# Performance work log

Hardware: AMD Instinct MI355X
Metric: run time of the kernel (lower is better)

## Reference

```python
import jax, jax.numpy as jnp
import numpy as np

N_NODES = 50000
N_EDGES = 800000
N_GRAPHS = 64
IN_C = 256      # num_commodities
HID = 256       # hidden_units
HID2 = HID // 2
N_DCS = 64


def setup_inputs() -> dict:
    key = jax.random.key(0)
    ks = jax.random.split(key, 8)
    x = jax.random.normal(ks[0], (N_NODES, IN_C), dtype=jnp.float32)
    edge_index = jax.random.randint(ks[1], (2, N_EDGES), 0, N_NODES, dtype=jnp.int32)
    # sorted graph-membership ids; even partition guarantees no empty graph
    batch = ((jnp.arange(N_NODES) * N_GRAPHS) // N_NODES).astype(jnp.int32)
    s1 = 1.0 / np.sqrt(IN_C)
    s2 = 1.0 / np.sqrt(HID)
    s3 = 1.0 / np.sqrt(HID2)
    W1 = jax.random.normal(ks[2], (IN_C, HID), dtype=jnp.float32) * s1
    b1 = jnp.zeros((HID,), dtype=jnp.float32)
    W2 = jax.random.normal(ks[3], (HID, HID2), dtype=jnp.float32) * s2
    b2 = jnp.zeros((HID2,), dtype=jnp.float32)
    Wm = jax.random.normal(ks[4], (HID2, N_DCS), dtype=jnp.float32) * s3
    bm = jax.random.normal(ks[5], (N_DCS,), dtype=jnp.float32) * s3
    return {"x": x, "edge_index": edge_index, "batch": batch,
            "W1": W1, "b1": b1, "W2": W2, "b2": b2, "Wm": Wm, "bm": bm}


def gcn_conv(x, W, b, src, dst, n_nodes):
    """PyG GCNConv: D^{-1/2}(A+I)D^{-1/2} X W + b (self-loops added)."""
    h = x @ W                                    # [N, out]
    ones = jnp.ones(src.shape[0], dtype=h.dtype)
    deg = jax.ops.segment_sum(ones, dst, num_segments=n_nodes) + 1.0  # +1 self-loop
    dis = jax.lax.rsqrt(deg)                     # deg >= 1, safe
    norm = dis[src] * dis[dst]                   # [E]
    agg = jax.ops.segment_sum(h[src] * norm[:, None], dst, num_segments=n_nodes)
    agg = agg + h * (dis * dis)[:, None]         # self-loop contribution
    return agg + b


def reference(x, edge_index, batch, W1, b1, W2, b2, Wm, bm):
    src, dst = edge_index[0], edge_index[1]
    n = x.shape[0]
    bx = jax.nn.relu(gcn_conv(x, W1, b1, src, dst, n))
    cx = jax.nn.relu(gcn_conv(bx, W2, b2, src, dst, n))
    px = jax.ops.segment_max(cx, batch, num_segments=N_GRAPHS)  # global max pool
    return px @ Wm + bm                           # [N_GRAPHS, N_DCS]
```

## Files before the change

kernel.cpp:

```cpp
#include <hip/hip_runtime.h>
#include <cstdint>


typedef _Float16 half2v __attribute__((ext_vector_type(2)));
typedef _Float16 half4v __attribute__((ext_vector_type(4)));
typedef _Float16 half8v __attribute__((ext_vector_type(8)));
typedef float f32x4 __attribute__((ext_vector_type(4)));

#define CAP 64

__device__ __forceinline__ void gl_lds16(const void* g, void* l) {
  __builtin_amdgcn_global_load_lds(
      (const __attribute__((address_space(1))) unsigned int*)g,
      (__attribute__((address_space(3))) unsigned int*)l, 16, 0, 0);
}

__global__ void cvtW_k(const float* __restrict__ W1, _Float16* __restrict__ Wt1,
                       const float* __restrict__ W2, _Float16* __restrict__ Wt2) {
  int i = blockIdx.x * 256 + threadIdx.x;
  if (i < 256 * 256) {
    int k = i >> 8, c = i & 255;
    Wt1[c * 256 + k] = (_Float16)W1[i];
  } else {
    int j = i - 256 * 256;
    if (j < 256 * 128) {
      int k = j >> 7, c = j & 127;
      Wt2[c * 256 + k] = (_Float16)W2[j];
    }
  }
}

__global__ void fill_slots_k(const int* __restrict__ src, const int* __restrict__ dst,
                             int* __restrict__ cnt, unsigned short* __restrict__ slots,
                             int E) {
  int e = blockIdx.x * blockDim.x + threadIdx.x;
  if (e >= E) return;
  int d = dst[e];
  int s = src[e];
  int p = atomicAdd(&cnt[d << 4], 1);
  if (p < CAP) slots[(d << 6) + p] = (unsigned short)s;
}

__global__ __launch_bounds__(256) void gemm1_k(const float* __restrict__ A,
                                               const _Float16* __restrict__ Bt,
                                               const int* __restrict__ cnt,
                                               _Float16* __restrict__ C, int M) {
  constexpr int K = 256, N = 256, BM = 32, BK = 32;
  __shared__ _Float16 As[BM * BK];
  __shared__ _Float16 Bs[N * BK];
  const int tid = threadIdx.x, lane = tid & 63, wave = tid >> 6;
  const int row0 = blockIdx.x * BM;
  const int kbase = (lane >> 4) * 8;
  const int r16 = lane & 15;

  const _Float16* bSrc[4];
  _Float16* bDst[4];
#pragma unroll
  for (int hh = 0; hh < 4; ++hh) {
    int fl = hh * 4 + wave;
    bSrc[hh] = Bt + (size_t)(fl * 16 + r16) * K + kbase;
    bDst[hh] = Bs + fl * 512;
  }

  const bool doA = tid < 128;
  const float* aSrc = nullptr;
  _Float16* aDst = nullptr;
  if (doA) {
    int arow = row0 + (tid >> 2);
    if (arow > M - 1) arow = M - 1;
    aSrc = A + (size_t)arow * K + (tid & 3) * 8;
    aDst = As + (tid >> 6) * 512 + (((tid & 3) << 4) + ((tid >> 2) & 15)) * 8;
  }

  f32x4 acc[2][4] = {};
  for (int k0 = 0; k0 < K; k0 += BK) {
#pragma unroll
    for (int hh = 0; hh < 4; ++hh) gl_lds16(bSrc[hh] + k0, bDst[hh]);
    if (doA) {
      float4 a0 = *(const float4*)(aSrc + k0);
      float4 a1 = *(const float4*)(aSrc + k0 + 4);
      half8v ah = {(_Float16)a0.x, (_Float16)a0.y, (_Float16)a0.z, (_Float16)a0.w,
                   (_Float16)a1.x, (_Float16)a1.y, (_Float16)a1.z, (_Float16)a1.w};
      *(half8v*)aDst = ah;
    }
    __syncthreads();

    half8v af[2], bf[4];
#pragma unroll
    for (int m = 0; m < 2; ++m)
      af[m] = *(const half8v*)(As + m * 512 + lane * 8);
#pragma unroll
    for (int nj = 0; nj < 4; ++nj)
      bf[nj] = *(const half8v*)(Bs + (wave * 4 + nj) * 512 + lane * 8);
#pragma unroll
    for (int m = 0; m < 2; ++m)
#pragma unroll
      for (int nj = 0; nj < 4; ++nj)
        acc[m][nj] = __builtin_amdgcn_mfma_f32_16x16x32_f16(af[m], bf[nj], acc[m][nj], 0, 0, 0);
    __syncthreads();
  }

#pragma unroll
  for (int m = 0; m < 2; ++m) {
    const int rbase = row0 + m * 16 + (lane >> 4) * 4;
    float dr[4];
#pragma unroll
    for (int r = 0; r < 4; ++r)
      dr[r] = (rbase + r < M) ? rsqrtf((float)cnt[(rbase + r) << 4] + 1.0f) : 0.f;
#pragma unroll
    for (int nj = 0; nj < 4; ++nj) {
      int col = wave * 64 + nj * 16 + r16;
#pragma unroll
      for (int r = 0; r < 4; ++r) {
        int row = rbase + r;
        if (row < M) C[(size_t)row * N + col] = (_Float16)(acc[m][nj][r] * dr[r]);
      }
    }
  }
}

__global__ __launch_bounds__(256) void gemm2_k(const _Float16* __restrict__ A,
                                               const _Float16* __restrict__ Bt,
                                               const int* __restrict__ cnt,
                                               _Float16* __restrict__ C, int M) {
  constexpr int K = 256, N = 128, BM = 32, BK = 32;
  __shared__ _Float16 As[BM * BK];
  __shared__ _Float16 Bs[N * BK];
  const int tid = threadIdx.x, lane = tid & 63, wave = tid >> 6;
  const int row0 = blockIdx.x * BM;
  const int kbase = (lane >> 4) * 8;
  const int r16 = lane & 15;

  const _Float16* bSrc[2];
  _Float16* bDst[2];
#pragma unroll
  for (int hh = 0; hh < 2; ++hh) {
    int fl = hh * 4 + wave;
    bSrc[hh] = Bt + (size_t)(fl * 16 + r16) * K + kbase;
    bDst[hh] = Bs + fl * 512;
  }

  const _Float16* aSrc = nullptr;
  _Float16* aDst = nullptr;
  if (wave < 2) {
    int arow = row0 + wave * 16 + r16;
    if (arow > M - 1) arow = M - 1;
    aSrc = A + (size_t)arow * K + kbase;
    aDst = As + wave * 512;
  }

  f32x4 acc[2][2] = {};
  for (int k0 = 0; k0 < K; k0 += BK) {
    gl_lds16(bSrc[0] + k0, bDst[0]);
    gl_lds16(bSrc[1] + k0, bDst[1]);
    if (wave < 2) gl_lds16(aSrc + k0, aDst);
    __syncthreads();

    half8v af[2], bf[2];
#pragma unroll
    for (int m = 0; m < 2; ++m)
      af[m] = *(const half8v*)(As + m * 512 + lane * 8);
#pragma unroll
    for (int j = 0; j < 2; ++j)
      bf[j] = *(const half8v*)(Bs + (wave * 2 + j) * 512 + lane * 8);
#pragma unroll
    for (int m = 0; m < 2; ++m)
#pragma unroll
      for (int j = 0; j < 2; ++j)
        acc[m][j] = __builtin_amdgcn_mfma_f32_16x16x32_f16(af[m], bf[j], acc[m][j], 0, 0, 0);
    __syncthreads();
  }

#pragma unroll
  for (int m = 0; m < 2; ++m) {
    const int rbase = row0 + m * 16 + (lane >> 4) * 4;
    float dr[4];
#pragma unroll
    for (int r = 0; r < 4; ++r)
      dr[r] = (rbase + r < M) ? rsqrtf((float)cnt[(rbase + r) << 4] + 1.0f) : 0.f;
#pragma unroll
    for (int j = 0; j < 2; ++j) {
      int col = wave * 32 + j * 16 + r16;
#pragma unroll
      for (int r = 0; r < 4; ++r) {
        int row = rbase + r;
        if (row < M) C[(size_t)row * N + col] = (_Float16)(acc[m][j][r] * dr[r]);
      }
    }
  }
}

template <int C, bool POOL>
__global__ __launch_bounds__(256) void agg_k(const _Float16* __restrict__ h,
                                             const int* __restrict__ cnt,
                                             const unsigned short* __restrict__ slots,
                                             const float* __restrict__ bias,
                                             const int* __restrict__ batch,
                                             void* __restrict__ outv, int n) {
  constexpr int LPR = C / 8;
  constexpr int EPW = 64 / LPR;
  constexpr int U = 8;
  constexpr int EBLK = EPW * U;
  const int tid = threadIdx.x;
  const int lane = tid & 63;
  const int wave = tid >> 6;
  const int slot = lane / LPR;
  const int ch0 = (lane % LPR) * 8;

  const int wid = blockIdx.x * 4 + wave;
  const bool valid = wid < n;
  const int node = valid ? wid : n - 1;

  const int rawc = cnt[node << 4];
  const int end = rawc < CAP ? rawc : CAP;
  const unsigned short* nsl = slots + (node << 6);

  float acc[8] = {};
  int jb = 0;
  for (; jb + EBLK <= end; jb += EBLK) {
    half2v ah0[4] = {}, ah1[4] = {};
#pragma unroll
    for (int u = 0; u < U; ++u) {
      int s = nsl[jb + u * EPW + slot];
      half8v hv = *(const half8v*)(h + (size_t)s * C + ch0);
      const half2v* hp = (const half2v*)&hv;
      if (u < 4) {
#pragma unroll
        for (int p = 0; p < 4; ++p) ah0[p] += hp[p];
      } else {
#pragma unroll
        for (int p = 0; p < 4; ++p) ah1[p] += hp[p];
      }
    }
#pragma unroll
    for (int p = 0; p < 4; ++p) {
      acc[2 * p + 0] += (float)ah0[p][0] + (float)ah1[p][0];
      acc[2 * p + 1] += (float)ah0[p][1] + (float)ah1[p][1];
    }
  }
  if (jb < end) {
    half2v ah0[4] = {}, ah1[4] = {};
#pragma unroll
    for (int u = 0; u < U; ++u) {
      int e = jb + u * EPW + slot;
      bool ok = e < end;
      int s = nsl[ok ? e : end - 1];
      half8v hv = *(const half8v*)(h + (size_t)s * C + ch0);
      if (!ok) hv = half8v{};
      const half2v* hp = (const half2v*)&hv;
      if (u < 4) {
#pragma unroll
        for (int p = 0; p < 4; ++p) ah0[p] += hp[p];
      } else {
#pragma unroll
        for (int p = 0; p < 4; ++p) ah1[p] += hp[p];
      }
    }
#pragma unroll
    for (int p = 0; p < 4; ++p) {
      acc[2 * p + 0] += (float)ah0[p][0] + (float)ah1[p][0];
      acc[2 * p + 1] += (float)ah0[p][1] + (float)ah1[p][1];
    }
  }

  if constexpr (EPW == 4) {
#pragma unroll
    for (int v = 0; v < 8; ++v) {
      acc[v] += __shfl_xor(acc[v], 16);
      acc[v] += __shfl_xor(acc[v], 32);
    }
  } else {
#pragma unroll
    for (int v = 0; v < 8; ++v) acc[v] += __shfl_xor(acc[v], 32);
  }

  const float di = rsqrtf((float)rawc + 1.0f);
  half8v sv = *(const half8v*)(h + (size_t)node * C + ch0);
  float4 blo = *(const float4*)(bias + ch0);
  float4 bhi = *(const float4*)(bias + ch0 + 4);
  const float bb[8] = {blo.x, blo.y, blo.z, blo.w, bhi.x, bhi.y, bhi.z, bhi.w};
  float res[8];
#pragma unroll
  for (int v = 0; v < 8; ++v)
    res[v] = fmaxf((acc[v] + (float)sv[v]) * di + bb[v], 0.f);

  if constexpr (!POOL) {
    if (valid && lane < LPR) {
      half8v r;
#pragma unroll
      for (int v = 0; v < 8; ++v) r[v] = (_Float16)res[v];
      *(half8v*)((_Float16*)outv + (size_t)node * C + ch0) = r;
    }
  } else {
    __shared__ float pres[4][C];
    __shared__ int pg[4];
    __shared__ int uni;
    const int g = valid ? batch[node] : -1 - wave;
    if (lane < LPR) {
      *(f32x4*)&pres[wave][ch0] = f32x4{res[0], res[1], res[2], res[3]};
      *(f32x4*)&pres[wave][ch0 + 4] = f32x4{res[4], res[5], res[6], res[7]};
    }
    if (lane == 0) pg[wave] = g;
    __syncthreads();
    if (tid == 0) uni = (pg[0] == pg[1] && pg[1] == pg[2] && pg[2] == pg[3] && pg[0] >= 0);
    __syncthreads();
    float* px = (float*)outv;
    if (uni) {
      if (tid < C) {
        float m = fmaxf(fmaxf(pres[0][tid], pres[1][tid]),
                        fmaxf(pres[2][tid], pres[3][tid]));
        atomicMax((int*)&px[(size_t)pg[0] * C + tid], __float_as_int(m));
      }
    } else {
#pragma unroll
      for (int wv = 0; wv < 4; ++wv) {
        int gg = pg[wv];
        if (gg >= 0 && tid < C)
          atomicMax((int*)&px[(size_t)gg * C + tid], __float_as_int(pres[wv][tid]));
      }
    }
  }
}

__global__ void final_mm_k(const float* __restrict__ px, const float* __restrict__ Wm,
                           const float* __restrict__ bm, float* __restrict__ out) {
  int g = blockIdx.x;
  int c = threadIdx.x;
  float acc = bm[c];
#pragma unroll 8
  for (int k = 0; k < 128; ++k)
    acc = fmaf(px[g * 128 + k], Wm[k * 64 + c], acc);
  out[g * 64 + c] = acc;
}

extern "C" void kernel_launch(void* const* d_in, const int* in_sizes, int n_in,
                              void* d_out, int out_size, void* d_ws, size_t ws_size,
                              hipStream_t stream) {
  const float* x     = (const float*)d_in[0];
  const int*   ei    = (const int*)d_in[1];
  const int*   batch = (const int*)d_in[2];
  const float* W1    = (const float*)d_in[3];
  const float* b1    = (const float*)d_in[4];
  const float* W2    = (const float*)d_in[5];
  const float* b2    = (const float*)d_in[6];
  const float* Wm    = (const float*)d_in[7];
  const float* bm    = (const float*)d_in[8];
  float* out = (float*)d_out;

  const int E = in_sizes[1] / 2;
  const int n = in_sizes[2];
  const int HID = 256, HID2 = 128, NG = 64;
  const int* src = ei;
  const int* dst = ei + E;

  char* w = (char*)d_ws;
  size_t off = 0;
  auto alloc = [&](size_t bytes) -> void* {
    void* p = w + off;
    off = (off + bytes + 255) & ~(size_t)255;
    return p;
  };
  int*            cnt    = (int*)alloc((size_t)n * 16 * 4);
  float*          px     = (float*)alloc((size_t)NG * HID2 * 4);
  size_t          zlen   = off;
  unsigned short* slots  = (unsigned short*)alloc((size_t)n * CAP * 2);
  _Float16*       Wt1    = (_Float16*)alloc((size_t)HID * 256 * 2);
  _Float16*       Wt2    = (_Float16*)alloc((size_t)HID2 * HID * 2);
  _Float16*       bufA   = (_Float16*)alloc((size_t)n * HID * 2);
  _Float16*       bufB   = (_Float16*)alloc((size_t)n * HID * 2);
  _Float16* h1 = bufA;
  _Float16* bx = bufB;
  _Float16* h2 = bufA;

  hipMemsetAsync(cnt, 0, zlen, stream);

  cvtW_k<<<(256 * 256 + 256 * 128 + 255) / 256, 256, 0, stream>>>(W1, Wt1, W2, Wt2);
  fill_slots_k<<<(E + 255) / 256, 256, 0, stream>>>(src, dst, cnt, slots, E);

  gemm1_k<<<(n + 31) / 32, 256, 0, stream>>>(x, Wt1, cnt, h1, n);
  agg_k<256, false><<<(n + 3) / 4, 256, 0, stream>>>(h1, cnt, slots, b1, nullptr, bx, n);

  gemm2_k<<<(n + 31) / 32, 256, 0, stream>>>(bx, Wt2, cnt, h2, n);
  agg_k<128, true><<<(n + 3) / 4, 256, 0, stream>>>(h2, cnt, slots, b2, batch, px, n);

  final_mm_k<<<NG, 64, 0, stream>>>(px, Wm, bm, out);
}
```

Measured before the change: 309.6 us.

## Store features in 32-channel column slices to shrink gather working set

GEMM outputs are now written in a channel-grouped layout, with each 32-channel slice stored contiguously for all nodes. Aggregation blocks each handle one slice, so random neighbour gathers touch only a per-slice working set (about 3.2MB) that fits in cache. Degree norms and clamped counts are precomputed into compact dis32/cnt8 arrays to avoid repeated rsqrt and strided count reads. The cost is more blocks, shorter 64-byte gathers, four-step shuffle reductions per node per slice, repeated slot-list reads per slice, and less coalesced GEMM output stores.

```diff
diff --git a/kernel.cpp b/kernel.cpp
--- a/kernel.cpp
+++ b/kernel.cpp
@@ -44,10 +44,13 @@
 __global__ __launch_bounds__(256) void gemm1_k(const float* __restrict__ A,
                                                const _Float16* __restrict__ Bt,
                                                const int* __restrict__ cnt,
-                                               _Float16* __restrict__ C, int M) {
-  constexpr int K = 256, N = 256, BM = 32, BK = 32;
+                                               _Float16* __restrict__ Cg,
+                                               float* __restrict__ dis32,
+                                               unsigned char* __restrict__ cnt8,
+                                               int M) {
+  constexpr int K = 256, BM = 32, BK = 32;
   __shared__ _Float16 As[BM * BK];
-  __shared__ _Float16 Bs[N * BK];
+  __shared__ _Float16 Bs[256 * BK];
   const int tid = threadIdx.x, lane = tid & 63, wave = tid >> 6;
   const int row0 = blockIdx.x * BM;
   const int kbase = (lane >> 4) * 8;
@@ -107,25 +110,38 @@
 #pragma unroll
     for (int r = 0; r < 4; ++r)
       dr[r] = (rbase + r < M) ? rsqrtf((float)cnt[(rbase + r) << 4] + 1.0f) : 0.f;
+    if (r16 == 0 && wave == 0) {
+#pragma unroll
+      for (int r = 0; r < 4; ++r) {
+        int row = rbase + r;
+        if (row < M) {
+          int rc = cnt[row << 4];
+          dis32[row] = dr[r];
+          cnt8[row] = (unsigned char)(rc < CAP ? rc : CAP);
+        }
+      }
+    }
 #pragma unroll
     for (int nj = 0; nj < 4; ++nj) {
       int col = wave * 64 + nj * 16 + r16;
+      int g = col >> 5, cg = col & 31;
 #pragma unroll
       for (int r = 0; r < 4; ++r) {
         int row = rbase + r;
-        if (row < M) C[(size_t)row * N + col] = (_Float16)(acc[m][nj][r] * dr[r]);
-      }
-    }
-  }
-}
-
-__global__ __launch_bounds__(256) void gemm2_k(const _Float16* __restrict__ A,
+        if (row < M)
+          Cg[((size_t)g * M + row) * 32 + cg] = (_Float16)(acc[m][nj][r] * dr[r]);
+      }
+    }
+  }
+}
+
+__global__ __launch_bounds__(256) void gemm2_k(const _Float16* __restrict__ Ag,
                                                const _Float16* __restrict__ Bt,
-                                               const int* __restrict__ cnt,
-                                               _Float16* __restrict__ C, int M) {
-  constexpr int K = 256, N = 128, BM = 32, BK = 32;
+                                               const float* __restrict__ dis32,
+                                               _Float16* __restrict__ Cg, int M) {
+  constexpr int K = 256, BM = 32, BK = 32;
   __shared__ _Float16 As[BM * BK];
-  __shared__ _Float16 Bs[N * BK];
+  __shared__ _Float16 Bs[128 * BK];
   const int tid = threadIdx.x, lane = tid & 63, wave = tid >> 6;
   const int row0 = blockIdx.x * BM;
   const int kbase = (lane >> 4) * 8;
@@ -140,12 +156,11 @@
     bDst[hh] = Bs + fl * 512;
   }
 
-  const _Float16* aSrc = nullptr;
+  int arow = 0;
   _Float16* aDst = nullptr;
   if (wave < 2) {
-    int arow = row0 + wave * 16 + r16;
+    arow = row0 + wave * 16 + r16;
     if (arow > M - 1) arow = M - 1;
-    aSrc = A + (size_t)arow * K + kbase;
     aDst = As + wave * 512;
   }
 
@@ -153,7 +168,8 @@
   for (int k0 = 0; k0 < K; k0 += BK) {
     gl_lds16(bSrc[0] + k0, bDst[0]);
     gl_lds16(bSrc[1] + k0, bDst[1]);
-    if (wave < 2) gl_lds16(aSrc + k0, aDst);
+    if (wave < 2)
+      gl_lds16(Ag + ((size_t)(k0 >> 5) * M + arow) * 32 + kbase, aDst);
     __syncthreads();
 
     half8v af[2], bf[2];
@@ -176,108 +192,68 @@
     const int rbase = row0 + m * 16 + (lane >> 4) * 4;
     float dr[4];
 #pragma unroll
-    for (int r = 0; r < 4; ++r)
-      dr[r] = (rbase + r < M) ? rsqrtf((float)cnt[(rbase + r) << 4] + 1.0f) : 0.f;
+    for (int r = 0; r < 4; ++r) dr[r] = (rbase + r < M) ? dis32[rbase + r] : 0.f;
 #pragma unroll
     for (int j = 0; j < 2; ++j) {
       int col = wave * 32 + j * 16 + r16;
+      int g = col >> 5, cg = col & 31;
 #pragma unroll
       for (int r = 0; r < 4; ++r) {
         int row = rbase + r;
-        if (row < M) C[(size_t)row * N + col] = (_Float16)(acc[m][j][r] * dr[r]);
-      }
-    }
-  }
-}
-
-template <int C, bool POOL>
-__global__ __launch_bounds__(256) void agg_k(const _Float16* __restrict__ h,
-                                             const int* __restrict__ cnt,
+        if (row < M)
+          Cg[((size_t)g * M + row) * 32 + cg] = (_Float16)(acc[m][j][r] * dr[r]);
+      }
+    }
+  }
+}
+
+template <int NGRP, bool POOL>
+__global__ __launch_bounds__(256) void agg_k(const _Float16* __restrict__ hg,
+                                             const float* __restrict__ dis32,
+                                             const unsigned char* __restrict__ cnt8,
                                              const unsigned short* __restrict__ slots,
                                              const float* __restrict__ bias,
                                              const int* __restrict__ batch,
                                              void* __restrict__ outv, int n) {
-  constexpr int LPR = C / 8;
-  constexpr int EPW = 64 / LPR;
-  constexpr int U = 8;
-  constexpr int EBLK = EPW * U;
   const int tid = threadIdx.x;
   const int lane = tid & 63;
   const int wave = tid >> 6;
-  const int slot = lane / LPR;
-  const int ch0 = (lane % LPR) * 8;
-
-  const int wid = blockIdx.x * 4 + wave;
+  const int g = blockIdx.x & (NGRP - 1);
+  const int chunk = blockIdx.x / NGRP;
+  const int slot = lane >> 2;
+  const int c8 = (lane & 3) * 8;
+
+  const int wid = chunk * 4 + wave;
   const bool valid = wid < n;
   const int node = valid ? wid : n - 1;
 
-  const int rawc = cnt[node << 4];
-  const int end = rawc < CAP ? rawc : CAP;
+  const int end = cnt8[node];
   const unsigned short* nsl = slots + (node << 6);
+  const _Float16* hslice = hg + (size_t)g * n * 32;
 
   float acc[8] = {};
-  int jb = 0;
-  for (; jb + EBLK <= end; jb += EBLK) {
-    half2v ah0[4] = {}, ah1[4] = {};
-#pragma unroll
-    for (int u = 0; u < U; ++u) {
-      int s = nsl[jb + u * EPW + slot];
-      half8v hv = *(const half8v*)(h + (size_t)s * C + ch0);
-      const half2v* hp = (const half2v*)&hv;
-      if (u < 4) {
-#pragma unroll
-        for (int p = 0; p < 4; ++p) ah0[p] += hp[p];
-      } else {
-#pragma unroll
-        for (int p = 0; p < 4; ++p) ah1[p] += hp[p];
-      }
-    }
-#pragma unroll
-    for (int p = 0; p < 4; ++p) {
-      acc[2 * p + 0] += (float)ah0[p][0] + (float)ah1[p][0];
-      acc[2 * p + 1] += (float)ah0[p][1] + (float)ah1[p][1];
-    }
-  }
-  if (jb < end) {
-    half2v ah0[4] = {}, ah1[4] = {};
-#pragma unroll
-    for (int u = 0; u < U; ++u) {
-      int e = jb + u * EPW + slot;
-      bool ok = e < end;
-      int s = nsl[ok ? e : end - 1];
-      half8v hv = *(const half8v*)(h + (size_t)s * C + ch0);
-      if (!ok) hv = half8v{};
-      const half2v* hp = (const half2v*)&hv;
-      if (u < 4) {
-#pragma unroll
-        for (int p = 0; p < 4; ++p) ah0[p] += hp[p];
-      } else {
-#pragma unroll
-        for (int p = 0; p < 4; ++p) ah1[p] += hp[p];
-      }
-    }
-#pragma unroll
-    for (int p = 0; p < 4; ++p) {
-      acc[2 * p + 0] += (float)ah0[p][0] + (float)ah1[p][0];
-      acc[2 * p + 1] += (float)ah0[p][1] + (float)ah1[p][1];
-    }
-  }
-
-  if constexpr (EPW == 4) {
-#pragma unroll
-    for (int v = 0; v < 8; ++v) {
-      acc[v] += __shfl_xor(acc[v], 16);
-      acc[v] += __shfl_xor(acc[v], 32);
-    }
-  } else {
-#pragma unroll
-    for (int v = 0; v < 8; ++v) acc[v] += __shfl_xor(acc[v], 32);
-  }
-
-  const float di = rsqrtf((float)rawc + 1.0f);
-  half8v sv = *(const half8v*)(h + (size_t)node * C + ch0);
-  float4 blo = *(const float4*)(bias + ch0);
-  float4 bhi = *(const float4*)(bias + ch0 + 4);
+  for (int jb = 0; jb < end; jb += 16) {
+    int e = jb + slot;
+    bool ok = e < end;
+    int s = nsl[ok ? e : 0];
+    half8v hv = *(const half8v*)(hslice + (size_t)s * 32 + c8);
+    if (!ok) hv = half8v{};
+#pragma unroll
+    for (int v = 0; v < 8; ++v) acc[v] += (float)hv[v];
+  }
+
+#pragma unroll
+  for (int v = 0; v < 8; ++v) {
+    acc[v] += __shfl_xor(acc[v], 4);
+    acc[v] += __shfl_xor(acc[v], 8);
+    acc[v] += __shfl_xor(acc[v], 16);
+    acc[v] += __shfl_xor(acc[v], 32);
+  }
+
+  const float di = dis32[node];
+  half8v sv = *(const half8v*)(hslice + (size_t)node * 32 + c8);
+  float4 blo = *(const float4*)(bias + g * 32 + c8);
+  float4 bhi = *(const float4*)(bias + g * 32 + c8 + 4);
   const float bb[8] = {blo.x, blo.y, blo.z, blo.w, bhi.x, bhi.y, bhi.z, bhi.w};
   float res[8];
 #pragma unroll
@@ -285,38 +261,39 @@
     res[v] = fmaxf((acc[v] + (float)sv[v]) * di + bb[v], 0.f);
 
   if constexpr (!POOL) {
-    if (valid && lane < LPR) {
+    if (valid && lane < 4) {
       half8v r;
 #pragma unroll
       for (int v = 0; v < 8; ++v) r[v] = (_Float16)res[v];
-      *(half8v*)((_Float16*)outv + (size_t)node * C + ch0) = r;
+      *(half8v*)((_Float16*)outv + ((size_t)g * n + node) * 32 + c8) = r;
     }
   } else {
-    __shared__ float pres[4][C];
+    __shared__ float pres[4][32];
     __shared__ int pg[4];
     __shared__ int uni;
-    const int g = valid ? batch[node] : -1 - wave;
-    if (lane < LPR) {
-      *(f32x4*)&pres[wave][ch0] = f32x4{res[0], res[1], res[2], res[3]};
-      *(f32x4*)&pres[wave][ch0 + 4] = f32x4{res[4], res[5], res[6], res[7]};
-    }
-    if (lane == 0) pg[wave] = g;
+    const int gb = valid ? batch[node] : -1 - wave;
+    if (lane < 4) {
+      *(f32x4*)&pres[wave][c8] = f32x4{res[0], res[1], res[2], res[3]};
+      *(f32x4*)&pres[wave][c8 + 4] = f32x4{res[4], res[5], res[6], res[7]};
+    }
+    if (lane == 0) pg[wave] = gb;
     __syncthreads();
     if (tid == 0) uni = (pg[0] == pg[1] && pg[1] == pg[2] && pg[2] == pg[3] && pg[0] >= 0);
     __syncthreads();
     float* px = (float*)outv;
     if (uni) {
-      if (tid < C) {
+      if (tid < 32) {
         float m = fmaxf(fmaxf(pres[0][tid], pres[1][tid]),
                         fmaxf(pres[2][tid], pres[3][tid]));
-        atomicMax((int*)&px[(size_t)pg[0] * C + tid], __float_as_int(m));
+        atomicMax((int*)&px[(size_t)pg[0] * 128 + g * 32 + tid], __float_as_int(m));
       }
     } else {
 #pragma unroll
       for (int wv = 0; wv < 4; ++wv) {
         int gg = pg[wv];
-        if (gg >= 0 && tid < C)
-          atomicMax((int*)&px[(size_t)gg * C + tid], __float_as_int(pres[wv][tid]));
+        if (gg >= 0 && tid < 32)
+          atomicMax((int*)&px[(size_t)gg * 128 + g * 32 + tid],
+                    __float_as_int(pres[wv][tid]));
       }
     }
   }
@@ -364,24 +341,28 @@
   float*          px     = (float*)alloc((size_t)NG * HID2 * 4);
   size_t          zlen   = off;
   unsigned short* slots  = (unsigned short*)alloc((size_t)n * CAP * 2);
+  float*          dis32  = (float*)alloc((size_t)n * 4);
+  unsigned char*  cnt8   = (unsigned char*)alloc((size_t)n);
   _Float16*       Wt1    = (_Float16*)alloc((size_t)HID * 256 * 2);
   _Float16*       Wt2    = (_Float16*)alloc((size_t)HID2 * HID * 2);
   _Float16*       bufA   = (_Float16*)alloc((size_t)n * HID * 2);
   _Float16*       bufB   = (_Float16*)alloc((size_t)n * HID * 2);
-  _Float16* h1 = bufA;
-  _Float16* bx = bufB;
-  _Float16* h2 = bufA;
+  _Float16* h1g = bufA;
+  _Float16* bxg = bufB;
+  _Float16* h2g = bufA;
 
   hipMemsetAsync(cnt, 0, zlen, stream);
 
   cvtW_k<<<(256 * 256 + 256 * 128 + 255) / 256, 256, 0, stream>>>(W1, Wt1, W2, Wt2);
   fill_slots_k<<<(E + 255) / 256, 256, 0, stream>>>(src, dst, cnt, slots, E);
 
-  gemm1_k<<<(n + 31) / 32, 256, 0, stream>>>(x, Wt1, cnt, h1, n);
-  agg_k<256, false><<<(n + 3) / 4, 256, 0, stream>>>(h1, cnt, slots, b1, nullptr, bx, n);
-
-  gemm2_k<<<(n + 31) / 32, 256, 0, stream>>>(bx, Wt2, cnt, h2, n);
-  agg_k<128, true><<<(n + 3) / 4, 256, 0, stream>>>(h2, cnt, slots, b2, batch, px, n);
+  gemm1_k<<<(n + 31) / 32, 256, 0, stream>>>(x, Wt1, cnt, h1g, dis32, cnt8, n);
+  agg_k<8, false><<<8 * ((n + 3) / 4), 256, 0, stream>>>(h1g, dis32, cnt8, slots,
+                                                         b1, nullptr, bxg, n);
+
+  gemm2_k<<<(n + 31) / 32, 256, 0, stream>>>(bxg, Wt2, dis32, h2g, n);
+  agg_k<4, true><<<4 * ((n + 3) / 4), 256, 0, stream>>>(h2g, dis32, cnt8, slots,
+                                                        b2, batch, px, n);
 
   final_mm_k<<<NG, 64, 0, stream>>>(px, Wm, bm, out);
 }
```

Result: slower. 437.5 us (+41.3%).
